# Performance work log

Measured on AMD Instinct MI355X. Metric: run time of the kernel, lower is better.

Reference implementation:

```python
import jax, jax.numpy as jnp
import numpy as np


def _diag_gather(x):
    # out[b,c,h,w] = x[b,c,h,(h+w)%W]; then transpose last two dims and flatten
    B, C, H, W = x.shape
    idx = (jnp.arange(H)[:, None] + jnp.arange(W)[None, :]) % W
    g = jnp.take_along_axis(x, idx[None, None], axis=3)  # [B,C,H,W]
    return g.transpose(0, 1, 3, 2).reshape(B, C, H * W)


def _antidiag_gather(x):
    B, C, H, W = x.shape
    idx = (jnp.arange(W)[None, :] - jnp.arange(H)[:, None]) % W
    g = jnp.take_along_axis(x, idx[None, None], axis=3)
    return g.transpose(0, 1, 3, 2).reshape(B, C, H * W)


def _diag_scatter(flat, shape):
    # exact inverse of _diag_gather (per-row circular-shift permutation)
    B, C, H, W = shape
    t = flat.reshape(B, C, W, H).transpose(0, 1, 3, 2)  # [B,C,H,W]
    inv = (jnp.arange(W)[None, :] - jnp.arange(H)[:, None]) % W
    return jnp.take_along_axis(t, inv[None, None], axis=3)


def _antidiag_scatter(flat, shape):
    B, C, H, W = shape
    t = flat.reshape(B, C, W, H).transpose(0, 1, 3, 2)
    inv = (jnp.arange(W)[None, :] + jnp.arange(H)[:, None]) % W
    return jnp.take_along_axis(t, inv[None, None], axis=3)


def cross_scan(x):
    # x: [B,C,H,W] -> xs: [B,8,C,L]; 8 scan directions (row, col, flips, diag, antidiag, flips)
    B, C, H, W = x.shape
    L = H * W
    xf = x.reshape(B, C, L)
    xt = x.transpose(0, 1, 3, 2).reshape(B, C, L)
    xd = _diag_gather(x)
    xa = _antidiag_gather(x)
    return jnp.stack(
        [xf, xt, xf[..., ::-1], xt[..., ::-1], xd, xa, xd[..., ::-1], xa[..., ::-1]],
        axis=1,
    )


def cross_merge(ys):
    # ys: [B,8,D,H,W] -> y: [B,D,L]
    B, K, D, H, W = ys.shape
    L = H * W
    ys = ys.reshape(B, K, D, L)
    a = ys[:, 0:2] + ys[:, 2:4][..., ::-1]
    y = a[:, 0] + a[:, 1].reshape(B, D, W, H).transpose(0, 1, 3, 2).reshape(B, D, L)
    b = ys[:, 4:6] + ys[:, 6:8][..., ::-1]
    y = y + _diag_scatter(b[:, 0], (B, D, H, W)).reshape(B, D, L)
    y = y + _antidiag_scatter(b[:, 1], (B, D, H, W)).reshape(B, D, L)
    return y


def selective_scan(u, delta, A, Bs, Cs, Ds):
    # u, delta: [B,KD,L]; A: [KD,N]; Bs, Cs: [B,K,N,L]; Ds: [KD]
    Bn, KD, L = u.shape
    K = Bs.shape[1]
    Dd = KD // K
    N = A.shape[1]
    dA = jnp.exp(delta[:, :, None, :] * A[None, :, :, None])  # [B,KD,N,L]
    Bexp = jnp.broadcast_to(Bs[:, :, None], (Bn, K, Dd, N, L)).reshape(Bn, KD, N, L)
    Cexp = jnp.broadcast_to(Cs[:, :, None], (Bn, K, Dd, N, L)).reshape(Bn, KD, N, L)
    dBu = delta[:, :, None, :] * Bexp * u[:, :, None, :]

    def comb(c1, c2):
        a1, b1 = c1
        a2, b2 = c2
        return a2 * a1, a2 * b1 + b2

    _, h = jax.lax.associative_scan(comb, (dA, dBu), axis=-1)  # h: [B,KD,N,L]
    return jnp.sum(Cexp * h, axis=2) + Ds[None, :, None] * u


def setup_inputs() -> dict:
    key = jax.random.key(0)
    ks = jax.random.split(key, 8)
    B, D, H, W = 1, 96, 64, 64
    K, N, R = 8, 16, 6
    return {
        "x": jax.random.normal(ks[0], (B, D, H, W), jnp.float32),
        "x_proj_weight": jax.random.normal(ks[1], (K, R + 2 * N, D), jnp.float32) * 0.05,
        "dt_projs_weight": jax.random.normal(ks[2], (K, D, R), jnp.float32) * 0.1,
        "dt_projs_bias": jax.random.normal(ks[3], (K, D), jnp.float32) * 0.1,
        "A_logs": jax.random.uniform(ks[4], (K * D, N), jnp.float32),
        "Ds": jax.random.normal(ks[5], (K * D,), jnp.float32),
        "out_norm_weight": jnp.ones((D,), jnp.float32),
        "out_norm_bias": jnp.zeros((D,), jnp.float32),
    }


def reference(x, x_proj_weight, dt_projs_weight, dt_projs_bias, A_logs, Ds,
              out_norm_weight, out_norm_bias):
    B, D, H, W = x.shape
    K, _, R = dt_projs_weight.shape
    N = A_logs.shape[1]
    L = H * W

    xs = cross_scan(x)  # [B,K,D,L]
    x_dbl = jnp.einsum("bkdl,kcd->bkcl", xs, x_proj_weight)  # [B,K,R+2N,L]
    dts, Bs, Cs = jnp.split(x_dbl, [R, R + N], axis=2)
    dts = jnp.einsum("bkrl,kdr->bkdl", dts, dt_projs_weight)  # [B,K,D,L]

    u = xs.reshape(B, K * D, L)
    delta = jax.nn.softplus(dts.reshape(B, K * D, L)
                            + dt_projs_bias.reshape(-1)[None, :, None])
    A = -jnp.exp(A_logs)  # [KD,N]

    ys = selective_scan(u, delta, A, Bs, Cs, Ds)  # [B,KD,L]
    y = cross_merge(ys.reshape(B, K, D, H, W))  # [B,D,L]

    # out_norm (v0): LayerNorm over channel dim
    y = y.transpose(0, 2, 1)  # [B,L,D]
    mu = jnp.mean(y, axis=-1, keepdims=True)
    var = jnp.var(y, axis=-1, keepdims=True)
    y = (y - mu) * jax.lax.rsqrt(var + 1e-5) * out_norm_weight + out_norm_bias
    return y.reshape(B, H, W, D)
```

## Files before the change

kernel.cpp:

```cpp
#include <hip/hip_runtime.h>
#include <math.h>

#define D_ 96
#define L_ 4096
#define K_ 8
#define N_ 16
#define R_ 6
#define CDBL 38
#define DL_ (D_ * L_)

#define REPN(M) M(0) M(1) M(2) M(3) M(4) M(5) M(6) M(7) \
                M(8) M(9) M(10) M(11) M(12) M(13) M(14) M(15)
#define REP8(M) M(0) M(1) M(2) M(3) M(4) M(5) M(6) M(7)
#define FENCE asm volatile("" ::: "memory");

#if __has_builtin(__builtin_amdgcn_exp2f)
#define EXP2(x) __builtin_amdgcn_exp2f(x)
#else
#define EXP2(x) exp2f(x)
#endif
#if __has_builtin(__builtin_amdgcn_logf)
#define LOG2F(x) __builtin_amdgcn_logf(x)
#else
#define LOG2F(x) __log2f(x)
#endif

#define LOG2E 1.44269504088896340736f
#define LN2F  0.69314718055994530942f

__device__ __forceinline__ int src_index(int k, int l) {
    int h = l & 63, w = l >> 6;
    int lp = 4095 - l;
    int hp = lp & 63, wp = lp >> 6;
    switch (k) {
    case 0: return l;
    case 1: return (h << 6) + w;
    case 2: return lp;
    case 3: return (hp << 6) + wp;
    case 4: return (h << 6) + ((h + w) & 63);
    case 5: return (h << 6) + ((w - h) & 63);
    case 6: return (hp << 6) + ((hp + wp) & 63);
    default: return (hp << 6) + ((wp - hp) & 63);
    }
}

__device__ __forceinline__ int merge_src(int k, int l) {
    int h = l >> 6, w = l & 63;
    int i1 = (w << 6) + h;
    int i4 = (((w - h) & 63) << 6) + h;
    int i5 = (((w + h) & 63) << 6) + h;
    switch (k) {
    case 0: return l;
    case 1: return i1;
    case 2: return 4095 - l;
    case 3: return 4095 - i1;
    case 4: return i4;
    case 5: return i5;
    case 6: return 4095 - i4;
    default: return 4095 - i5;
    }
}

#define PQ(p) ((((p) >> 6) * 66) + ((p) & 63))

__global__ __launch_bounds__(256) void k_xscan(const float* __restrict__ x,
                                               float* __restrict__ xs) {
    __shared__ float img[64 * 66];
    int bid = blockIdx.x;
    int k = bid & 7;
    int d = bid >> 3;
    int t = threadIdx.x;
    const float* xd = x + d * L_;
    #pragma unroll
    for (int i = 0; i < 16; ++i) {
        int l = i * 256 + t;
        img[PQ(l)] = xd[l];
    }
    __syncthreads();
    float* dst = xs + (k * D_ + d) * L_;
    #pragma unroll
    for (int i = 0; i < 16; ++i) {
        int l = i * 256 + t;
        dst[l] = img[PQ(src_index(k, l))];
    }
}

__global__ __launch_bounds__(256) void k_xdbl(const float* __restrict__ xs,
                                              const float* __restrict__ wproj,
                                              float* __restrict__ xdbl) {
    __shared__ float tile[64][100];
    int bid = blockIdx.x;
    int swz = (bid & 7) * 64 + (bid >> 3);
    int k = swz >> 6;
    int l0 = (swz & 63) * 64;

    const float* src = xs + k * DL_ + l0;
    for (int e = threadIdx.x; e < D_ * 64; e += 256) {
        int d = e >> 6, li = e & 63;
        tile[li][d] = src[d * L_ + li];
    }
    __syncthreads();

    int lt = threadIdx.x & 63;
    int cg = __builtin_amdgcn_readfirstlane(threadIdx.x >> 6);
    const float* wk = wproj + k * CDBL * D_;
    float acc[10];
    #pragma unroll
    for (int j = 0; j < 10; ++j) acc[j] = 0.f;
    for (int d4 = 0; d4 < D_; d4 += 4) {
        float4 tv = *(const float4*)&tile[lt][d4];
        #pragma unroll
        for (int j = 0; j < 10; ++j) {
            int c = cg + 4 * j;
            if (c < CDBL) {
                float4 wv = *(const float4*)&wk[c * D_ + d4];
                acc[j] = fmaf(tv.x, wv.x, acc[j]);
                acc[j] = fmaf(tv.y, wv.y, acc[j]);
                acc[j] = fmaf(tv.z, wv.z, acc[j]);
                acc[j] = fmaf(tv.w, wv.w, acc[j]);
            }
        }
    }
    #pragma unroll
    for (int j = 0; j < 10; ++j) {
        int c = cg + 4 * j;
        if (c < CDBL) xdbl[(k * CDBL + c) * L_ + l0 + lt] = acc[j];
    }
}


#if __has_builtin(__builtin_amdgcn_update_dpp)
#define HAVE_DPP 1
template<int CTRL, int RM>
__device__ __forceinline__ float updpp(float oldv, float src) {
    int r = __builtin_amdgcn_update_dpp(__builtin_bit_cast(int, oldv),
                                        __builtin_bit_cast(int, src),
                                        CTRL, RM, 0xF, false);
    return __builtin_bit_cast(float, r);
}
#else
#define HAVE_DPP 0
#endif

__global__ __launch_bounds__(256, 3) void k_scan(const float* __restrict__ xdbl,
                                                 const float* __restrict__ dtw,
                                                 const float* __restrict__ dtb,
                                                 const float* __restrict__ alogs,
                                                 const float* __restrict__ dsv_,
                                                 const float* __restrict__ xs,
                                                 float* __restrict__ ys) {
    int bid = blockIdx.x;
    int k = bid & 7;
    int d = bid >> 3;
    int kd = k * D_ + d;
    int t = threadIdx.x;
    int lane = t & 63, wv = t >> 6;
    int l0t = t * 16;

    __shared__ float An_s[16];
    __shared__ float agg_a[4][16], agg_b[4][16];
    __shared__ float cb_s[4][16];
    if (t < 16)
        An_s[t] = -expf(alogs[kd * N_ + t]);

#define DECL(n) float sA##n, sB##n;
    REPN(DECL)
#undef DECL
#define DECL(i) float d##i, u##i, y##i;
    REPN(DECL)
#undef DECL

    const float* xr = xdbl + k * CDBL * L_;
    const float2* wp2 = (const float2*)(dtw + kd * R_);
    const float2 w01 = wp2[0], w23 = wp2[1], w45 = wp2[2];
    const float bias = dtb[kd];
    const float dval = dsv_[kd];
#define SPL2(dst, s) { float p = (s) * LOG2E; \
    float l2 = LOG2F(1.f + EXP2(p)); \
    dst = ((s) > 20.f) ? p : l2; }
#define DLTQ(j, i0, i1, i2, i3) { \
    const float4 r0 = *(const float4*)(xr + 0 * L_ + l0t + j * 4); \
    const float4 r1 = *(const float4*)(xr + 1 * L_ + l0t + j * 4); \
    const float4 r2 = *(const float4*)(xr + 2 * L_ + l0t + j * 4); \
    const float4 r3 = *(const float4*)(xr + 3 * L_ + l0t + j * 4); \
    const float4 r4 = *(const float4*)(xr + 4 * L_ + l0t + j * 4); \
    const float4 r5 = *(const float4*)(xr + 5 * L_ + l0t + j * 4); \
    float s; \
    s = fmaf(w01.x, r0.x, bias); s = fmaf(w01.y, r1.x, s); s = fmaf(w23.x, r2.x, s); \
    s = fmaf(w23.y, r3.x, s); s = fmaf(w45.x, r4.x, s); s = fmaf(w45.y, r5.x, s); \
    SPL2(d##i0, s) \
    s = fmaf(w01.x, r0.y, bias); s = fmaf(w01.y, r1.y, s); s = fmaf(w23.x, r2.y, s); \
    s = fmaf(w23.y, r3.y, s); s = fmaf(w45.x, r4.y, s); s = fmaf(w45.y, r5.y, s); \
    SPL2(d##i1, s) \
    s = fmaf(w01.x, r0.z, bias); s = fmaf(w01.y, r1.z, s); s = fmaf(w23.x, r2.z, s); \
    s = fmaf(w23.y, r3.z, s); s = fmaf(w45.x, r4.z, s); s = fmaf(w45.y, r5.z, s); \
    SPL2(d##i2, s) \
    s = fmaf(w01.x, r0.w, bias); s = fmaf(w01.y, r1.w, s); s = fmaf(w23.x, r2.w, s); \
    s = fmaf(w23.y, r3.w, s); s = fmaf(w45.x, r4.w, s); s = fmaf(w45.y, r5.w, s); \
    SPL2(d##i3, s) }
    DLTQ(0, 0, 1, 2, 3)   FENCE
    DLTQ(1, 4, 5, 6, 7)   FENCE
    DLTQ(2, 8, 9, 10, 11) FENCE
    DLTQ(3, 12, 13, 14, 15)
#undef DLTQ
#undef SPL2

    {
        const float* up = xs + kd * L_ + l0t;
        const float4 ua = *(const float4*)(up);
        const float4 ub = *(const float4*)(up + 4);
        const float4 uc = *(const float4*)(up + 8);
        const float4 ud = *(const float4*)(up + 12);
        u0 = ua.x; u1 = ua.y; u2 = ua.z; u3 = ua.w;
        u4 = ub.x; u5 = ub.y; u6 = ub.z; u7 = ub.w;
        u8 = uc.x; u9 = uc.y; u10 = uc.z; u11 = uc.w;
        u12 = ud.x; u13 = ud.y; u14 = ud.z; u15 = ud.w;
    }
#define UG(i) y##i = dval * u##i; u##i *= LN2F; u##i *= d##i;
    REPN(UG)
#undef UG

    __syncthreads();

    const float* Bptr = xdbl + (k * CDBL + R_) * L_ + l0t;
    const float* Cptr = Bptr + N_ * L_;

#define PHA_E(i, Bc) { float e = EXP2(d##i * An); \
    rb = fmaf(e, rb, u##i * (Bc)); ra *= e; }
#define PHA(n) { \
    const float An = An_s[n]; \
    const float* Bn = Bptr + n * L_; \
    const float4 b0 = *(const float4*)(Bn), b1 = *(const float4*)(Bn + 4); \
    const float4 b2 = *(const float4*)(Bn + 8), b3 = *(const float4*)(Bn + 12); \
    float ra = 1.f, rb = 0.f; \
    PHA_E(0, b0.x) PHA_E(1, b0.y) PHA_E(2, b0.z) PHA_E(3, b0.w) \
    PHA_E(4, b1.x) PHA_E(5, b1.y) PHA_E(6, b1.z) PHA_E(7, b1.w) \
    PHA_E(8, b2.x) PHA_E(9, b2.y) PHA_E(10, b2.z) PHA_E(11, b2.w) \
    PHA_E(12, b3.x) PHA_E(13, b3.y) PHA_E(14, b3.z) PHA_E(15, b3.w) \
    sA##n = ra; sB##n = rb; \
    FENCE }
    REPN(PHA)
#undef PHA
#undef PHA_E

#if HAVE_DPP
#define SSTN(n) { float pa = updpp<SC_CTRL, SC_RM>(1.f, sA##n); \
                  float pb = updpp<SC_CTRL, SC_RM>(0.f, sB##n); \
                  sB##n = fmaf(sA##n, pb, sB##n); sA##n *= pa; }
#define SC_CTRL 0x111
#define SC_RM 0xF
    REPN(SSTN)
#undef SC_CTRL
#undef SC_RM
#define SC_CTRL 0x112
#define SC_RM 0xF
    REPN(SSTN)
#undef SC_CTRL
#undef SC_RM
#define SC_CTRL 0x114
#define SC_RM 0xF
    REPN(SSTN)
#undef SC_CTRL
#undef SC_RM
#define SC_CTRL 0x118
#define SC_RM 0xF
    REPN(SSTN)
#undef SC_CTRL
#undef SC_RM
#define SC_CTRL 0x142
#define SC_RM 0xA
    REPN(SSTN)
#undef SC_CTRL
#undef SC_RM
#define SC_CTRL 0x143
#define SC_RM 0xC
    REPN(SSTN)
#undef SC_CTRL
#undef SC_RM
#undef SSTN

#define PPREF(n) { \
    if (lane == 63) { agg_a[wv][n] = sA##n; agg_b[wv][n] = sB##n; } \
    sA##n = updpp<0x138, 0xF>(1.f, sA##n); \
    sB##n = updpp<0x138, 0xF>(0.f, sB##n); }
    REPN(PPREF)
#undef PPREF
#else
#define PBF(n) { float pa = __shfl_up(sA##n, off); float pb = __shfl_up(sB##n, off); \
    if (lane >= off) { sB##n = fmaf(sA##n, pb, sB##n); sA##n *= pa; } }
    for (int off = 1; off < 64; off <<= 1) { REPN(PBF) }
#undef PBF
#define PPREF(n) { float ia = sA##n, ib = sB##n; \
    float ea = __shfl_up(ia, 1); float eb = __shfl_up(ib, 1); \
    if (lane == 0) { ea = 1.f; eb = 0.f; } \
    if (lane == 63) { agg_a[wv][n] = ia; agg_b[wv][n] = ib; } \
    sA##n = ea; sB##n = eb; }
    REPN(PPREF)
#undef PPREF
#endif
    __syncthreads();

    if (t < 64) {
        int w = t >> 4, n = t & 15;
        float cb = 0.f;
        for (int w2 = 0; w2 < w; ++w2)
            cb = fmaf(agg_a[w2][n], cb, agg_b[w2][n]);
        cb_s[w][n] = cb;
    }
    __syncthreads();
#define PC(n) { sA##n = fmaf(sA##n, cb_s[wv][n], sB##n); }
    REPN(PC)
#undef PC

#define PHD_E(i, Bc, Cc) { float e = EXP2(d##i * An); \
    h = fmaf(e, h, u##i * (Bc)); y##i = fmaf((Cc), h, y##i); }
#define PHD(n) { \
    const float An = An_s[n]; float h = sA##n; \
    const float* Bn = Bptr + n * L_; const float* Cn = Cptr + n * L_; \
    const float4 b0 = *(const float4*)(Bn), b1 = *(const float4*)(Bn + 4); \
    const float4 b2 = *(const float4*)(Bn + 8), b3 = *(const float4*)(Bn + 12); \
    const float4 c0 = *(const float4*)(Cn), c1 = *(const float4*)(Cn + 4); \
    const float4 c2 = *(const float4*)(Cn + 8), c3 = *(const float4*)(Cn + 12); \
    PHD_E(0, b0.x, c0.x) PHD_E(1, b0.y, c0.y) PHD_E(2, b0.z, c0.z) PHD_E(3, b0.w, c0.w) \
    PHD_E(4, b1.x, c1.x) PHD_E(5, b1.y, c1.y) PHD_E(6, b1.z, c1.z) PHD_E(7, b1.w, c1.w) \
    PHD_E(8, b2.x, c2.x) PHD_E(9, b2.y, c2.y) PHD_E(10, b2.z, c2.z) PHD_E(11, b2.w, c2.w) \
    PHD_E(12, b3.x, c3.x) PHD_E(13, b3.y, c3.y) PHD_E(14, b3.z, c3.z) PHD_E(15, b3.w, c3.w) \
    FENCE }
    REPN(PHD)
#undef PHD
#undef PHD_E

    float* yp = ys + kd * L_ + l0t;
    {
        float4 o;
        o.x = y0;  o.y = y1;  o.z = y2;  o.w = y3;  *(float4*)(yp + 0)  = o;
        o.x = y4;  o.y = y5;  o.z = y6;  o.w = y7;  *(float4*)(yp + 4)  = o;
        o.x = y8;  o.y = y9;  o.z = y10; o.w = y11; *(float4*)(yp + 8)  = o;
        o.x = y12; o.y = y13; o.z = y14; o.w = y15; *(float4*)(yp + 12) = o;
    }
}

__global__ __launch_bounds__(512) void k_merge(const float* __restrict__ ys,
                                               float* __restrict__ ym2) {
    __shared__ float buf[64 * 66];
    int bid = blockIdx.x;
    int kg = bid & 1;
    int d = bid >> 1;
    int t = threadIdx.x;
    float a0 = 0.f, a1 = 0.f, a2 = 0.f, a3 = 0.f,
          a4 = 0.f, a5 = 0.f, a6 = 0.f, a7 = 0.f;
    #pragma unroll
    for (int kk = 0; kk < 4; ++kk) {
        int k = kg * 4 + kk;
        const float* srow = ys + (k * D_ + d) * L_;
        #pragma unroll
        for (int i = 0; i < 8; ++i) {
            int l = i * 512 + t;
            buf[PQ(l)] = srow[l];
        }
        __syncthreads();
#define MACC(i) { int l = i * 512 + t; a##i += buf[PQ(merge_src(k, l))]; }
        REP8(MACC)
#undef MACC
        __syncthreads();
    }
    float* drow = ym2 + (kg * D_ + d) * L_;
#define MST(i) drow[i * 512 + t] = a##i;
    REP8(MST)
#undef MST
}

__global__ __launch_bounds__(256) void k_ln(const float* __restrict__ ym2,
                                            const float* __restrict__ gamma,
                                            const float* __restrict__ beta,
                                            float* __restrict__ out) {
    __shared__ float tile[D_][17];
    __shared__ float pS[16][17], pQ[16][17];
    __shared__ float mu_s[16], rs_s[16];
    int t = threadIdx.x;
    int lb = blockIdx.x * 16;

    #pragma unroll
    for (int i = 0; i < 6; ++i) {
        int e = i * 256 + t;
        int dd = e >> 4, ll = e & 15;
        float v = ym2[dd * L_ + lb + ll] + ym2[DL_ + dd * L_ + lb + ll];
        tile[dd][ll] = v;
    }
    __syncthreads();
    {
        int g = t >> 4, ll = t & 15;
        float s = 0.f, sq = 0.f;
        #pragma unroll
        for (int j = 0; j < 6; ++j) {
            float v = tile[g * 6 + j][ll];
            s += v; sq = fmaf(v, v, sq);
        }
        pS[g][ll] = s; pQ[g][ll] = sq;
    }
    __syncthreads();
    if (t < 16) {
        float s = 0.f, sq = 0.f;
        #pragma unroll
        for (int g = 0; g < 16; ++g) { s += pS[g][t]; sq += pQ[g][t]; }
        float mu = s * (1.f / 96.f);
        float var = sq * (1.f / 96.f) - mu * mu;
        mu_s[t] = mu;
        rs_s[t] = rsqrtf(var + 1e-5f);
    }
    __syncthreads();
    #pragma unroll
    for (int i = 0; i < 6; ++i) {
        int e = i * 256 + t;
        int ll = e / 96, dd = e - ll * 96;
        float v = tile[dd][ll];
        float o = fmaf((v - mu_s[ll]) * rs_s[ll], gamma[dd], beta[dd]);
        out[lb * 96 + e] = o;
    }
}

extern "C" void kernel_launch(void* const* d_in, const int* in_sizes, int n_in,
                              void* d_out, int out_size, void* d_ws, size_t ws_size,
                              hipStream_t stream) {
    const float* x     = (const float*)d_in[0];
    const float* wproj = (const float*)d_in[1];
    const float* dtw   = (const float*)d_in[2];
    const float* dtb   = (const float*)d_in[3];
    const float* alogs = (const float*)d_in[4];
    const float* dsv   = (const float*)d_in[5];
    const float* gamma = (const float*)d_in[6];
    const float* beta  = (const float*)d_in[7];
    float* out = (float*)d_out;
    float* ws  = (float*)d_ws;

    float* xs   = ws;
    float* xdbl = ws + 3145728;
    float* ym2  = ws + 4390912;

    hipLaunchKernelGGL(k_xscan, dim3(768), dim3(256), 0, stream, x, xs);
    hipLaunchKernelGGL(k_xdbl, dim3(512), dim3(256), 0, stream, xs, wproj, xdbl);
    hipLaunchKernelGGL(k_scan, dim3(768), dim3(256), 0, stream,
                       xdbl, dtw, dtb, alogs, dsv, xs, xs );
    hipLaunchKernelGGL(k_merge, dim3(192), dim3(512), 0, stream, xs, ym2);
    hipLaunchKernelGGL(k_ln, dim3(256), dim3(256), 0, stream, ym2, gamma, beta, out);
}
```

Measured before the change: 101.9 us.

## Halve per-thread sequence chunk in scan kernel, doubling threads per block

The selective-scan kernel now uses 512 threads per block, each handling 8 timesteps instead of 16. The cross-wave carry combine grows from 4 to 8 waves to match. Per-thread register state shrinks, which aims to raise occupancy and latency hiding on the exp-heavy sequential loops. The cost is a larger DPP/shuffle scan and carry phase relative to the work done per thread, and the compiler fences are regrouped.

```diff
diff --git a/kernel.cpp b/kernel.cpp
--- a/kernel.cpp
+++ b/kernel.cpp
@@ -142,7 +142,7 @@
 #define HAVE_DPP 0
 #endif
 
-__global__ __launch_bounds__(256, 3) void k_scan(const float* __restrict__ xdbl,
+__global__ __launch_bounds__(512, 3) void k_scan(const float* __restrict__ xdbl,
                                                  const float* __restrict__ dtw,
                                                  const float* __restrict__ dtb,
                                                  const float* __restrict__ alogs,
@@ -155,11 +155,11 @@
     int kd = k * D_ + d;
     int t = threadIdx.x;
     int lane = t & 63, wv = t >> 6;
-    int l0t = t * 16;
+    int l0t = t * 8;
 
     __shared__ float An_s[16];
-    __shared__ float agg_a[4][16], agg_b[4][16];
-    __shared__ float cb_s[4][16];
+    __shared__ float agg_a[8][16], agg_b[8][16];
+    __shared__ float cb_s[8][16];
     if (t < 16)
         An_s[t] = -expf(alogs[kd * N_ + t]);
 
@@ -167,7 +167,7 @@
     REPN(DECL)
 #undef DECL
 #define DECL(i) float d##i, u##i, y##i;
-    REPN(DECL)
+    REP8(DECL)
 #undef DECL
 
     const float* xr = xdbl + k * CDBL * L_;
@@ -198,10 +198,8 @@
     s = fmaf(w01.x, r0.w, bias); s = fmaf(w01.y, r1.w, s); s = fmaf(w23.x, r2.w, s); \
     s = fmaf(w23.y, r3.w, s); s = fmaf(w45.x, r4.w, s); s = fmaf(w45.y, r5.w, s); \
     SPL2(d##i3, s) }
-    DLTQ(0, 0, 1, 2, 3)   FENCE
-    DLTQ(1, 4, 5, 6, 7)   FENCE
-    DLTQ(2, 8, 9, 10, 11) FENCE
-    DLTQ(3, 12, 13, 14, 15)
+    DLTQ(0, 0, 1, 2, 3)
+    DLTQ(1, 4, 5, 6, 7)
 #undef DLTQ
 #undef SPL2
 
@@ -209,15 +207,11 @@
         const float* up = xs + kd * L_ + l0t;
         const float4 ua = *(const float4*)(up);
         const float4 ub = *(const float4*)(up + 4);
-        const float4 uc = *(const float4*)(up + 8);
-        const float4 ud = *(const float4*)(up + 12);
         u0 = ua.x; u1 = ua.y; u2 = ua.z; u3 = ua.w;
         u4 = ub.x; u5 = ub.y; u6 = ub.z; u7 = ub.w;
-        u8 = uc.x; u9 = uc.y; u10 = uc.z; u11 = uc.w;
-        u12 = ud.x; u13 = ud.y; u14 = ud.z; u15 = ud.w;
     }
 #define UG(i) y##i = dval * u##i; u##i *= LN2F; u##i *= d##i;
-    REPN(UG)
+    REP8(UG)
 #undef UG
 
     __syncthreads();
@@ -231,15 +225,14 @@
     const float An = An_s[n]; \
     const float* Bn = Bptr + n * L_; \
     const float4 b0 = *(const float4*)(Bn), b1 = *(const float4*)(Bn + 4); \
-    const float4 b2 = *(const float4*)(Bn + 8), b3 = *(const float4*)(Bn + 12); \
     float ra = 1.f, rb = 0.f; \
     PHA_E(0, b0.x) PHA_E(1, b0.y) PHA_E(2, b0.z) PHA_E(3, b0.w) \
     PHA_E(4, b1.x) PHA_E(5, b1.y) PHA_E(6, b1.z) PHA_E(7, b1.w) \
-    PHA_E(8, b2.x) PHA_E(9, b2.y) PHA_E(10, b2.z) PHA_E(11, b2.w) \
-    PHA_E(12, b3.x) PHA_E(13, b3.y) PHA_E(14, b3.z) PHA_E(15, b3.w) \
-    sA##n = ra; sB##n = rb; \
-    FENCE }
-    REPN(PHA)
+    sA##n = ra; sB##n = rb; }
+    PHA(0) PHA(1) PHA(2) PHA(3) FENCE
+    PHA(4) PHA(5) PHA(6) PHA(7) FENCE
+    PHA(8) PHA(9) PHA(10) PHA(11) FENCE
+    PHA(12) PHA(13) PHA(14) PHA(15) FENCE
 #undef PHA
 #undef PHA_E
 
@@ -300,7 +293,7 @@
 #endif
     __syncthreads();
 
-    if (t < 64) {
+    if (t < 128) {
         int w = t >> 4, n = t & 15;
         float cb = 0.f;
         for (int w2 = 0; w2 < w; ++w2)
@@ -318,25 +311,25 @@
     const float An = An_s[n]; float h = sA##n; \
     const float* Bn = Bptr + n * L_; const float* Cn = Cptr + n * L_; \
     const float4 b0 = *(const float4*)(Bn), b1 = *(const float4*)(Bn + 4); \
-    const float4 b2 = *(const float4*)(Bn + 8), b3 = *(const float4*)(Bn + 12); \
     const float4 c0 = *(const float4*)(Cn), c1 = *(const float4*)(Cn + 4); \
-    const float4 c2 = *(const float4*)(Cn + 8), c3 = *(const float4*)(Cn + 12); \
     PHD_E(0, b0.x, c0.x) PHD_E(1, b0.y, c0.y) PHD_E(2, b0.z, c0.z) PHD_E(3, b0.w, c0.w) \
-    PHD_E(4, b1.x, c1.x) PHD_E(5, b1.y, c1.y) PHD_E(6, b1.z, c1.z) PHD_E(7, b1.w, c1.w) \
-    PHD_E(8, b2.x, c2.x) PHD_E(9, b2.y, c2.y) PHD_E(10, b2.z, c2.z) PHD_E(11, b2.w, c2.w) \
-    PHD_E(12, b3.x, c3.x) PHD_E(13, b3.y, c3.y) PHD_E(14, b3.z, c3.z) PHD_E(15, b3.w, c3.w) \
-    FENCE }
-    REPN(PHD)
+    PHD_E(4, b1.x, c1.x) PHD_E(5, b1.y, c1.y) PHD_E(6, b1.z, c1.z) PHD_E(7, b1.w, c1.w) }
+    PHD(0) PHD(1) FENCE
+    PHD(2) PHD(3) FENCE
+    PHD(4) PHD(5) FENCE
+    PHD(6) PHD(7) FENCE
+    PHD(8) PHD(9) FENCE
+    PHD(10) PHD(11) FENCE
+    PHD(12) PHD(13) FENCE
+    PHD(14) PHD(15) FENCE
 #undef PHD
 #undef PHD_E
 
     float* yp = ys + kd * L_ + l0t;
     {
         float4 o;
-        o.x = y0;  o.y = y1;  o.z = y2;  o.w = y3;  *(float4*)(yp + 0)  = o;
-        o.x = y4;  o.y = y5;  o.z = y6;  o.w = y7;  *(float4*)(yp + 4)  = o;
-        o.x = y8;  o.y = y9;  o.z = y10; o.w = y11; *(float4*)(yp + 8)  = o;
-        o.x = y12; o.y = y13; o.z = y14; o.w = y15; *(float4*)(yp + 12) = o;
+        o.x = y0; o.y = y1; o.z = y2; o.w = y3; *(float4*)(yp + 0) = o;
+        o.x = y4; o.y = y5; o.z = y6; o.w = y7; *(float4*)(yp + 4) = o;
     }
 }
 
@@ -439,7 +432,7 @@
 
     hipLaunchKernelGGL(k_xscan, dim3(768), dim3(256), 0, stream, x, xs);
     hipLaunchKernelGGL(k_xdbl, dim3(512), dim3(256), 0, stream, xs, wproj, xdbl);
-    hipLaunchKernelGGL(k_scan, dim3(768), dim3(256), 0, stream,
+    hipLaunchKernelGGL(k_scan, dim3(768), dim3(512), 0, stream,
                        xdbl, dtw, dtb, alogs, dsv, xs, xs );
     hipLaunchKernelGGL(k_merge, dim3(192), dim3(512), 0, stream, xs, ym2);
     hipLaunchKernelGGL(k_ln, dim3(256), dim3(256), 0, stream, ym2, gamma, beta, out);
```

Result: faster. 89.43 us (median of 2 runs) (-12.3%).
